# Kernel optimization log

Hardware: AMD Instinct MI355X
Metric: run time of the kernel (lower is better)

Reference implementation:

```python
import jax, jax.numpy as jnp
import numpy as np

N_NODES = 100000


def _deg_isqrt(idx, n):
    # clamped-to-1 degree, then ^-0.5 (DGL GraphConv norm='both')
    deg = jax.ops.segment_sum(jnp.ones(idx.shape, jnp.float32), idx, num_segments=n)
    return jnp.power(jnp.maximum(deg, 1.0), -0.5)


def _graph_conv(feat, W, b, src, dst, out_isqrt, in_isqrt, n):
    # norm='both': scale by src out-degree^-1/2, mult-first (in>out), spmm, scale by dst in-degree^-1/2
    h = (feat * out_isqrt[:, None]) @ W                      # [N, out]
    h = jax.ops.segment_sum(h[src], dst, num_segments=n)     # gather/scatter over edges
    return h * in_isqrt[:, None] + b


def setup_inputs() -> dict:
    key = jax.random.key(0)
    ks = jax.random.split(key, 10)
    in_dim, h1, h2 = 512, 64, 32
    n, e = N_NODES, 800000
    features = jax.random.normal(ks[0], (n, in_dim), jnp.float32)
    src = jax.random.randint(ks[1], (e,), 0, n)
    dst = jax.random.randint(ks[2], (e,), 0, n)
    noise = jax.random.normal(ks[3], (n, h2), jnp.float32)
    s1 = 1.0 / np.sqrt(in_dim)
    s2 = 1.0 / np.sqrt(h1)
    W1 = jax.random.uniform(ks[4], (in_dim, h1), jnp.float32, -s1, s1)
    b1 = jnp.zeros((h1,), jnp.float32)
    W2 = jax.random.uniform(ks[5], (h1, h2), jnp.float32, -s2, s2)
    b2 = jnp.zeros((h2,), jnp.float32)
    W3 = jax.random.uniform(ks[6], (h1, h2), jnp.float32, -s2, s2)
    b3 = jnp.zeros((h2,), jnp.float32)
    return {"features": features, "src": src, "dst": dst, "noise": noise,
            "W1": W1, "b1": b1, "W2": W2, "b2": b2, "W3": W3, "b3": b3}


def reference(features, src, dst, noise, W1, b1, W2, b2, W3, b3):
    n = features.shape[0]
    out_isqrt = _deg_isqrt(src, n)
    in_isqrt = _deg_isqrt(dst, n)
    h = jax.nn.relu(_graph_conv(features, W1, b1, src, dst, out_isqrt, in_isqrt, n))
    mean = _graph_conv(h, W2, b2, src, dst, out_isqrt, in_isqrt, n)
    log_std = _graph_conv(h, W3, b3, src, dst, out_isqrt, in_isqrt, n)
    z = mean + noise * jnp.exp(log_std)
    return z, mean, log_std
```

## Files before the change

kernel.cpp:

```cpp
#include <hip/hip_runtime.h>
#include <hip/hip_bf16.h>


typedef __attribute__((ext_vector_type(8))) short short8;
typedef __attribute__((ext_vector_type(4))) float f32x4;

static __device__ inline short f2bf(float f)
{
    union { __hip_bfloat16 h; short s; } u;
    u.h = __float2bfloat16(f);
    return u.s;
}

static __device__ inline short8 cvt8(float4 lo, float4 hi)
{
    short8 r;
    r[0] = f2bf(lo.x); r[1] = f2bf(lo.y); r[2] = f2bf(lo.z); r[3] = f2bf(lo.w);
    r[4] = f2bf(hi.x); r[5] = f2bf(hi.y); r[6] = f2bf(hi.z); r[7] = f2bf(hi.w);
    return r;
}

__global__ __launch_bounds__(256) void k_pack_w1(
    const float* __restrict__ W1, short* __restrict__ w1f)
{
    int gid = blockIdx.x * 256 + threadIdx.x;
    if (gid >= 512 * 64) return;
    int k = gid >> 6, c = gid & 63;
    int kt = k >> 5, kk = k & 31, nt = c >> 4, lr = c & 15;
    int kg = kk >> 3, j = kk & 7;
    int l = kg * 16 + lr;
    w1f[(kt * 4 + nt) * 512 + l * 8 + j] = f2bf(W1[gid]);
}

__global__ __launch_bounds__(256) void k_build_wc(
    const float* __restrict__ W2, const float* __restrict__ W3,
    float* __restrict__ wc)
{
    int gid = blockIdx.x * 256 + threadIdx.x;
    if (gid >= 64 * 64) return;
    int k = gid >> 6, c = gid & 63;
    wc[gid] = (c < 32) ? W2[k * 32 + c] : W3[k * 32 + (c - 32)];
}

__global__ __launch_bounds__(256) void k_deg_int(
    const int* __restrict__ src, const int* __restrict__ dst,
    int* __restrict__ degS, int* __restrict__ degD, int e)
{
    int gid = blockIdx.x * 256 + threadIdx.x;
    if (gid >= e) return;
    atomicAdd(&degS[src[gid]], 1);
    atomicAdd(&degD[dst[gid]], 1);
}

__global__ __launch_bounds__(256) void k_scan_block_sums(
    const int* __restrict__ deg, int* __restrict__ partials, int n)
{
    __shared__ int red[256];
    int gid = blockIdx.x * 256 + threadIdx.x;
    red[threadIdx.x] = (gid < n) ? deg[gid] : 0;
    __syncthreads();
    for (int s = 128; s > 0; s >>= 1) {
        if (threadIdx.x < s) red[threadIdx.x] += red[threadIdx.x + s];
        __syncthreads();
    }
    if (threadIdx.x == 0) partials[blockIdx.x] = red[0];
}

__global__ __launch_bounds__(512) void k_scan_partials(
    int* __restrict__ partials, int nb)
{
    __shared__ int s[512];
    int t = threadIdx.x;
    s[t] = (t < nb) ? partials[t] : 0;
    __syncthreads();
    for (int d = 1; d < 512; d <<= 1) {
        int v = (t >= d) ? s[t - d] : 0;
        __syncthreads();
        s[t] += v;
        __syncthreads();
    }
    if (t < nb) partials[t] = (t == 0) ? 0 : s[t - 1];
}

__global__ __launch_bounds__(256) void k_scan_final(
    const int* __restrict__ degD, const int* __restrict__ degS,
    const int* __restrict__ partials,
    int* __restrict__ row_ptr, int* __restrict__ cursor,
    float* __restrict__ isq_out, float* __restrict__ isq_in, int n)
{
    __shared__ int s[256];
    int t = threadIdx.x;
    int gid = blockIdx.x * 256 + t;
    int v = (gid < n) ? degD[gid] : 0;
    s[t] = v;
    __syncthreads();
    for (int d = 1; d < 256; d <<= 1) {
        int u = (t >= d) ? s[t - d] : 0;
        __syncthreads();
        s[t] += u;
        __syncthreads();
    }
    int start = partials[blockIdx.x] + s[t] - v;
    if (gid < n) {
        row_ptr[gid] = start;
        cursor[gid]  = start;
        isq_in[gid]  = 1.0f / sqrtf((float)max(v, 1));
        isq_out[gid] = 1.0f / sqrtf((float)max(degS[gid], 1));
    }
    if (gid == n - 1) row_ptr[n] = start + v;
}

__global__ __launch_bounds__(256) void k_scatter(
    const int* __restrict__ src, const int* __restrict__ dst,
    int* __restrict__ cursor, int* __restrict__ edge_src, int e)
{
    int gid = blockIdx.x * 256 + threadIdx.x;
    if (gid >= e) return;
    int pos = atomicAdd(&cursor[dst[gid]], 1);
    edge_src[pos] = src[gid];
}

__global__ __launch_bounds__(256) void k_gemm1_mfma(
    const float* __restrict__ X, const short* __restrict__ w1f,
    const float* __restrict__ scale, float* __restrict__ Y, int n)
{
    const int tid  = threadIdx.x;
    const int l    = tid & 63;
    const int wv   = tid >> 6;
    const int row0 = blockIdx.x * 128 + wv * 32;
    const int lr   = l & 15;
    const int kg   = l >> 4;

    int ra0 = row0 + lr;       if (ra0 >= n) ra0 = n - 1;
    int ra1 = row0 + 16 + lr;  if (ra1 >= n) ra1 = n - 1;
    const float* pa0 = X + (size_t)ra0 * 512 + kg * 8;
    const float* pa1 = X + (size_t)ra1 * 512 + kg * 8;

    f32x4 acc[2][4];
#pragma unroll
    for (int i = 0; i < 2; ++i)
#pragma unroll
        for (int j = 0; j < 4; ++j) acc[i][j] = (f32x4){0.f, 0.f, 0.f, 0.f};

    float4 a0lo = *(const float4*)(pa0);
    float4 a0hi = *(const float4*)(pa0 + 4);
    float4 a1lo = *(const float4*)(pa1);
    float4 a1hi = *(const float4*)(pa1 + 4);

    for (int kt = 0; kt < 16; ++kt) {
        const short* pb = w1f + (size_t)(kt * 4) * 512 + l * 8;
        short8 b0 = *(const short8*)(pb);
        short8 b1 = *(const short8*)(pb + 512);
        short8 b2 = *(const short8*)(pb + 1024);
        short8 b3 = *(const short8*)(pb + 1536);

        short8 a0 = cvt8(a0lo, a0hi);
        short8 a1 = cvt8(a1lo, a1hi);

        if (kt < 15) {
            const float* q0 = pa0 + (kt + 1) * 32;
            const float* q1 = pa1 + (kt + 1) * 32;
            a0lo = *(const float4*)(q0);
            a0hi = *(const float4*)(q0 + 4);
            a1lo = *(const float4*)(q1);
            a1hi = *(const float4*)(q1 + 4);
        }

        acc[0][0] = __builtin_amdgcn_mfma_f32_16x16x32_bf16(a0, b0, acc[0][0], 0, 0, 0);
        acc[0][1] = __builtin_amdgcn_mfma_f32_16x16x32_bf16(a0, b1, acc[0][1], 0, 0, 0);
        acc[0][2] = __builtin_amdgcn_mfma_f32_16x16x32_bf16(a0, b2, acc[0][2], 0, 0, 0);
        acc[0][3] = __builtin_amdgcn_mfma_f32_16x16x32_bf16(a0, b3, acc[0][3], 0, 0, 0);
        acc[1][0] = __builtin_amdgcn_mfma_f32_16x16x32_bf16(a1, b0, acc[1][0], 0, 0, 0);
        acc[1][1] = __builtin_amdgcn_mfma_f32_16x16x32_bf16(a1, b1, acc[1][1], 0, 0, 0);
        acc[1][2] = __builtin_amdgcn_mfma_f32_16x16x32_bf16(a1, b2, acc[1][2], 0, 0, 0);
        acc[1][3] = __builtin_amdgcn_mfma_f32_16x16x32_bf16(a1, b3, acc[1][3], 0, 0, 0);
    }

#pragma unroll
    for (int mr = 0; mr < 2; ++mr) {
#pragma unroll
        for (int m = 0; m < 4; ++m) {
            int row = row0 + mr * 16 + kg * 4 + m;
            if (row < n) {
                float s = scale[row];
#pragma unroll
                for (int nt = 0; nt < 4; ++nt)
                    Y[(size_t)row * 64 + nt * 16 + lr] = acc[mr][nt][m] * s;
            }
        }
    }
}

__global__ __launch_bounds__(256) void k_gemm2(
    const float* __restrict__ X, const float* __restrict__ W,
    float* __restrict__ Y, int n)
{
    __shared__ float sx[64][68];
    __shared__ float sw[64][64];
    const int tid  = threadIdx.x;
    const int colp = tid & 31;
    const int rg   = tid >> 5;
    const int row0 = blockIdx.x * 64;

    float2 acc[8];
#pragma unroll
    for (int i = 0; i < 8; ++i) acc[i] = make_float2(0.f, 0.f);

#pragma unroll
    for (int p = 0; p < 4; ++p) {
        int u = p * 256 + tid;
        int r = u >> 4, c4 = (u & 15) * 4;
        int row = row0 + r;
        float4 v = make_float4(0.f, 0.f, 0.f, 0.f);
        if (row < n) v = *(const float4*)&X[(size_t)row * 64 + c4];
        *(float4*)&sx[r][c4] = v;
        *(float4*)&sw[r][c4] = *(const float4*)&W[u * 4];
    }
    __syncthreads();

#pragma unroll 4
    for (int k4 = 0; k4 < 64; k4 += 4) {
        float2 w0 = *(const float2*)&sw[k4 + 0][colp * 2];
        float2 w1 = *(const float2*)&sw[k4 + 1][colp * 2];
        float2 w2 = *(const float2*)&sw[k4 + 2][colp * 2];
        float2 w3 = *(const float2*)&sw[k4 + 3][colp * 2];
#pragma unroll
        for (int i = 0; i < 8; ++i) {
            float4 f = *(const float4*)&sx[rg * 8 + i][k4];
            acc[i].x += f.x * w0.x + f.y * w1.x + f.z * w2.x + f.w * w3.x;
            acc[i].y += f.x * w0.y + f.y * w1.y + f.z * w2.y + f.w * w3.y;
        }
    }

#pragma unroll
    for (int i = 0; i < 8; ++i) {
        int row = row0 + rg * 8 + i;
        if (row < n)
            *(float2*)&Y[(size_t)row * 64 + colp * 2] =
                make_float2(acc[i].x, acc[i].y);
    }
}

__global__ __launch_bounds__(256) void k_gather_h(
    const int* __restrict__ row_ptr, const int* __restrict__ edge_src,
    const float* __restrict__ x, const float* __restrict__ isq_in,
    const float* __restrict__ isq_out, const float* __restrict__ b1,
    float* __restrict__ h, int n)
{
    int col  = threadIdx.x & 63;
    int node = __builtin_amdgcn_readfirstlane(blockIdx.x * 4 + (threadIdx.x >> 6));
    if (node >= n) return;
    int j = row_ptr[node], jend = row_ptr[node + 1];
    float a0 = 0.f, a1 = 0.f, a2 = 0.f, a3 = 0.f;
    for (; j + 3 < jend; j += 4) {
        int e0 = edge_src[j], e1 = edge_src[j + 1];
        int e2 = edge_src[j + 2], e3 = edge_src[j + 3];
        a0 += x[(size_t)e0 * 64 + col];
        a1 += x[(size_t)e1 * 64 + col];
        a2 += x[(size_t)e2 * 64 + col];
        a3 += x[(size_t)e3 * 64 + col];
    }
    for (; j < jend; ++j) a0 += x[(size_t)edge_src[j] * 64 + col];
    float acc = (a0 + a1) + (a2 + a3);
    h[(size_t)node * 64 + col] =
        fmaxf(acc * isq_in[node] + b1[col], 0.f) * isq_out[node];
}

__global__ __launch_bounds__(256) void k_gather_final(
    const int* __restrict__ row_ptr, const int* __restrict__ edge_src,
    const float* __restrict__ t23, const float* __restrict__ isq_in,
    const float* __restrict__ b2, const float* __restrict__ b3,
    const float* __restrict__ noise, float* __restrict__ out, int n)
{
    int lane = threadIdx.x & 63;
    int node = __builtin_amdgcn_readfirstlane(blockIdx.x * 4 + (threadIdx.x >> 6));
    if (node >= n) return;
    int j = row_ptr[node], jend = row_ptr[node + 1];
    float a0 = 0.f, a1 = 0.f, a2 = 0.f, a3 = 0.f;
    for (; j + 3 < jend; j += 4) {
        int e0 = edge_src[j], e1 = edge_src[j + 1];
        int e2 = edge_src[j + 2], e3 = edge_src[j + 3];
        a0 += t23[(size_t)e0 * 64 + lane];
        a1 += t23[(size_t)e1 * 64 + lane];
        a2 += t23[(size_t)e2 * 64 + lane];
        a3 += t23[(size_t)e3 * 64 + lane];
    }
    for (; j < jend; ++j) a0 += t23[(size_t)edge_src[j] * 64 + lane];
    float acc = (a0 + a1) + (a2 + a3);
    float si = isq_in[node];
    float v  = acc * si + (lane < 32 ? b2[lane] : b3[lane - 32]);
    float lv = __shfl(v, lane | 32, 64);
    int total = n * 32;
    int base  = node * 32 + (lane & 31);
    if (lane < 32) {
        float z = v + noise[base] * expf(lv);
        out[base]         = z;
        out[total + base] = v;
    } else {
        out[2 * total + base] = v;
    }
}

extern "C" void kernel_launch(void* const* d_in, const int* in_sizes, int n_in,
                              void* d_out, int out_size, void* d_ws, size_t ws_size,
                              hipStream_t stream)
{
    const float* feat  = (const float*)d_in[0];
    const int*   src   = (const int*)d_in[1];
    const int*   dst   = (const int*)d_in[2];
    const float* noise = (const float*)d_in[3];
    const float* W1    = (const float*)d_in[4];
    const float* b1    = (const float*)d_in[5];
    const float* W2    = (const float*)d_in[6];
    const float* b2    = (const float*)d_in[7];
    const float* W3    = (const float*)d_in[8];
    const float* b3    = (const float*)d_in[9];

    const int n = in_sizes[0] / 512;
    const int e = in_sizes[1];

    float* ws      = (float*)d_ws;
    float* isq_out = ws;
    float* isq_in  = ws + n;
    float* bufA    = ws + 2 * (size_t)n;
    float* bufB    = bufA + 64 * (size_t)n;
    float* wc      = bufB + 64 * (size_t)n;
    short* w1f     = (short*)(wc + 64 * 64);
    int*   ip      = (int*)(w1f + 512 * 64);
    int* row_ptr   = ip;
    int* cursor    = ip + (n + 1);
    int* partials  = cursor + n;
    int* edge_src  = partials + 512;
    int* degS = (int*)bufA;
    int* degD = degS + n;
    float* out = (float*)d_out;

    const int nb = (n + 255) / 256;

    hipMemsetAsync(degS, 0, 2 * (size_t)n * sizeof(int), stream);

    k_build_wc<<<(64 * 64 + 255) / 256, 256, 0, stream>>>(W2, W3, wc);
    k_pack_w1<<<(512 * 64 + 255) / 256, 256, 0, stream>>>(W1, w1f);
    k_deg_int<<<(e + 255) / 256, 256, 0, stream>>>(src, dst, degS, degD, e);

    k_scan_block_sums<<<nb, 256, 0, stream>>>(degD, partials, n);
    k_scan_partials<<<1, 512, 0, stream>>>(partials, nb);
    k_scan_final<<<nb, 256, 0, stream>>>(
        degD, degS, partials, row_ptr, cursor, isq_out, isq_in, n);
    k_scatter<<<(e + 255) / 256, 256, 0, stream>>>(src, dst, cursor, edge_src, e);

    k_gemm1_mfma<<<(n + 127) / 128, 256, 0, stream>>>(
        feat, w1f, isq_out, bufA, n);

    k_gather_h<<<(n + 3) / 4, 256, 0, stream>>>(
        row_ptr, edge_src, bufA, isq_in, isq_out, b1, bufB, n);

    k_gemm2<<<(n + 63) / 64, 256, 0, stream>>>(bufB, wc, bufA, n);

    k_gather_final<<<(n + 3) / 4, 256, 0, stream>>>(
        row_ptr, edge_src, bufA, isq_in, b2, b3, noise, out, n);
}
```

Measured before the change: 305.1 us.

## Store per-node projected features in bf16 and widen gather unroll

The GEMM outputs (the layer-1 projection and the layer-2/3 projections) are now written as bf16 instead of fp32. This halves the bytes moved by the two edge-gather kernels, which widen to fp32 on load and now unroll eight edges per iteration. The change also merges the weight packing, the wc build and the degree memset into one setup kernel, and software-pipelines the B-fragment loads in the MFMA GEMM. Rounding the intermediates to bf16 reduces accuracy, and the setup kernel zeroes 2n/4 int4 values, which leaves the tail of degS unzeroed when 2n is not a multiple of 4.

New measurement: 282.0 us. -7.6%, faster.

```diff
diff --git a/kernel.cpp b/kernel.cpp
--- a/kernel.cpp
+++ b/kernel.cpp
@@ -4,12 +4,20 @@
 
 typedef __attribute__((ext_vector_type(8))) short short8;
 typedef __attribute__((ext_vector_type(4))) float f32x4;
+typedef unsigned short ushort_t;
 
 static __device__ inline short f2bf(float f)
 {
     union { __hip_bfloat16 h; short s; } u;
     u.h = __float2bfloat16(f);
     return u.s;
+}
+
+static __device__ inline float bf2f(ushort_t u)
+{
+    union { float f; unsigned v; } w;
+    w.v = ((unsigned)u) << 16;
+    return w.f;
 }
 
 static __device__ inline short8 cvt8(float4 lo, float4 hi)
@@ -20,26 +28,24 @@
     return r;
 }
 
-__global__ __launch_bounds__(256) void k_pack_w1(
-    const float* __restrict__ W1, short* __restrict__ w1f)
+__global__ __launch_bounds__(256) void k_setup(
+    const float* __restrict__ W1, const float* __restrict__ W2,
+    const float* __restrict__ W3, short* __restrict__ w1f,
+    float* __restrict__ wc, int4* __restrict__ zp, int z4)
 {
     int gid = blockIdx.x * 256 + threadIdx.x;
-    if (gid >= 512 * 64) return;
-    int k = gid >> 6, c = gid & 63;
-    int kt = k >> 5, kk = k & 31, nt = c >> 4, lr = c & 15;
-    int kg = kk >> 3, j = kk & 7;
-    int l = kg * 16 + lr;
-    w1f[(kt * 4 + nt) * 512 + l * 8 + j] = f2bf(W1[gid]);
-}
-
-__global__ __launch_bounds__(256) void k_build_wc(
-    const float* __restrict__ W2, const float* __restrict__ W3,
-    float* __restrict__ wc)
-{
-    int gid = blockIdx.x * 256 + threadIdx.x;
-    if (gid >= 64 * 64) return;
-    int k = gid >> 6, c = gid & 63;
-    wc[gid] = (c < 32) ? W2[k * 32 + c] : W3[k * 32 + (c - 32)];
+    if (gid < z4) zp[gid] = make_int4(0, 0, 0, 0);
+    if (gid < 64 * 64) {
+        int k = gid >> 6, c = gid & 63;
+        wc[gid] = (c < 32) ? W2[k * 32 + c] : W3[k * 32 + (c - 32)];
+    }
+    if (gid < 512 * 64) {
+        int k = gid >> 6, c = gid & 63;
+        int kt = k >> 5, kk = k & 31, nt = c >> 4, lr = c & 15;
+        int kg = kk >> 3, j = kk & 7;
+        int l = kg * 16 + lr;
+        w1f[(kt * 4 + nt) * 512 + l * 8 + j] = f2bf(W1[gid]);
+    }
 }
 
 __global__ __launch_bounds__(256) void k_deg_int(
@@ -122,7 +128,7 @@
 
 __global__ __launch_bounds__(256) void k_gemm1_mfma(
     const float* __restrict__ X, const short* __restrict__ w1f,
-    const float* __restrict__ scale, float* __restrict__ Y, int n)
+    const float* __restrict__ scale, ushort_t* __restrict__ Y, int n)
 {
     const int tid  = threadIdx.x;
     const int l    = tid & 63;
@@ -135,6 +141,7 @@
     int ra1 = row0 + 16 + lr;  if (ra1 >= n) ra1 = n - 1;
     const float* pa0 = X + (size_t)ra0 * 512 + kg * 8;
     const float* pa1 = X + (size_t)ra1 * 512 + kg * 8;
+    const short* pb  = w1f + l * 8;
 
     f32x4 acc[2][4];
 #pragma unroll
@@ -146,16 +153,15 @@
     float4 a0hi = *(const float4*)(pa0 + 4);
     float4 a1lo = *(const float4*)(pa1);
     float4 a1hi = *(const float4*)(pa1 + 4);
+    short8 b0 = *(const short8*)(pb);
+    short8 b1 = *(const short8*)(pb + 512);
+    short8 b2 = *(const short8*)(pb + 1024);
+    short8 b3 = *(const short8*)(pb + 1536);
 
     for (int kt = 0; kt < 16; ++kt) {
-        const short* pb = w1f + (size_t)(kt * 4) * 512 + l * 8;
-        short8 b0 = *(const short8*)(pb);
-        short8 b1 = *(const short8*)(pb + 512);
-        short8 b2 = *(const short8*)(pb + 1024);
-        short8 b3 = *(const short8*)(pb + 1536);
-
-        short8 a0 = cvt8(a0lo, a0hi);
-        short8 a1 = cvt8(a1lo, a1hi);
+        short8 ca0 = cvt8(a0lo, a0hi);
+        short8 ca1 = cvt8(a1lo, a1hi);
+        short8 cb0 = b0, cb1 = b1, cb2 = b2, cb3 = b3;
 
         if (kt < 15) {
             const float* q0 = pa0 + (kt + 1) * 32;
@@ -164,16 +170,21 @@
             a0hi = *(const float4*)(q0 + 4);
             a1lo = *(const float4*)(q1);
             a1hi = *(const float4*)(q1 + 4);
+            const short* q = pb + (size_t)(kt + 1) * 2048;
+            b0 = *(const short8*)(q);
+            b1 = *(const short8*)(q + 512);
+            b2 = *(const short8*)(q + 1024);
+            b3 = *(const short8*)(q + 1536);
         }
 
-        acc[0][0] = __builtin_amdgcn_mfma_f32_16x16x32_bf16(a0, b0, acc[0][0], 0, 0, 0);
-        acc[0][1] = __builtin_amdgcn_mfma_f32_16x16x32_bf16(a0, b1, acc[0][1], 0, 0, 0);
-        acc[0][2] = __builtin_amdgcn_mfma_f32_16x16x32_bf16(a0, b2, acc[0][2], 0, 0, 0);
-        acc[0][3] = __builtin_amdgcn_mfma_f32_16x16x32_bf16(a0, b3, acc[0][3], 0, 0, 0);
-        acc[1][0] = __builtin_amdgcn_mfma_f32_16x16x32_bf16(a1, b0, acc[1][0], 0, 0, 0);
-        acc[1][1] = __builtin_amdgcn_mfma_f32_16x16x32_bf16(a1, b1, acc[1][1], 0, 0, 0);
-        acc[1][2] = __builtin_amdgcn_mfma_f32_16x16x32_bf16(a1, b2, acc[1][2], 0, 0, 0);
-        acc[1][3] = __builtin_amdgcn_mfma_f32_16x16x32_bf16(a1, b3, acc[1][3], 0, 0, 0);
+        acc[0][0] = __builtin_amdgcn_mfma_f32_16x16x32_bf16(ca0, cb0, acc[0][0], 0, 0, 0);
+        acc[0][1] = __builtin_amdgcn_mfma_f32_16x16x32_bf16(ca0, cb1, acc[0][1], 0, 0, 0);
+        acc[0][2] = __builtin_amdgcn_mfma_f32_16x16x32_bf16(ca0, cb2, acc[0][2], 0, 0, 0);
+        acc[0][3] = __builtin_amdgcn_mfma_f32_16x16x32_bf16(ca0, cb3, acc[0][3], 0, 0, 0);
+        acc[1][0] = __builtin_amdgcn_mfma_f32_16x16x32_bf16(ca1, cb0, acc[1][0], 0, 0, 0);
+        acc[1][1] = __builtin_amdgcn_mfma_f32_16x16x32_bf16(ca1, cb1, acc[1][1], 0, 0, 0);
+        acc[1][2] = __builtin_amdgcn_mfma_f32_16x16x32_bf16(ca1, cb2, acc[1][2], 0, 0, 0);
+        acc[1][3] = __builtin_amdgcn_mfma_f32_16x16x32_bf16(ca1, cb3, acc[1][3], 0, 0, 0);
     }
 
 #pragma unroll
@@ -185,15 +196,53 @@
                 float s = scale[row];
 #pragma unroll
                 for (int nt = 0; nt < 4; ++nt)
-                    Y[(size_t)row * 64 + nt * 16 + lr] = acc[mr][nt][m] * s;
+                    Y[(size_t)row * 64 + nt * 16 + lr] =
+                        (ushort_t)f2bf(acc[mr][nt][m] * s);
             }
         }
     }
 }
 
+__global__ __launch_bounds__(256) void k_gather_h(
+    const int* __restrict__ row_ptr, const int* __restrict__ edge_src,
+    const ushort_t* __restrict__ x, const float* __restrict__ isq_in,
+    const float* __restrict__ isq_out, const float* __restrict__ b1,
+    float* __restrict__ h, int n)
+{
+    int col  = threadIdx.x & 63;
+    int node = __builtin_amdgcn_readfirstlane(blockIdx.x * 4 + (threadIdx.x >> 6));
+    if (node >= n) return;
+    int j = row_ptr[node], jend = row_ptr[node + 1];
+    float a0 = 0.f, a1 = 0.f, a2 = 0.f, a3 = 0.f;
+    float a4 = 0.f, a5 = 0.f, a6 = 0.f, a7 = 0.f;
+    for (; j + 7 < jend; j += 8) {
+        int e0 = edge_src[j],     e1 = edge_src[j + 1];
+        int e2 = edge_src[j + 2], e3 = edge_src[j + 3];
+        int e4 = edge_src[j + 4], e5 = edge_src[j + 5];
+        int e6 = edge_src[j + 6], e7 = edge_src[j + 7];
+        a0 += bf2f(x[(size_t)e0 * 64 + col]);
+        a1 += bf2f(x[(size_t)e1 * 64 + col]);
+        a2 += bf2f(x[(size_t)e2 * 64 + col]);
+        a3 += bf2f(x[(size_t)e3 * 64 + col]);
+        a4 += bf2f(x[(size_t)e4 * 64 + col]);
+        a5 += bf2f(x[(size_t)e5 * 64 + col]);
+        a6 += bf2f(x[(size_t)e6 * 64 + col]);
+        a7 += bf2f(x[(size_t)e7 * 64 + col]);
+    }
+    for (; j + 1 < jend; j += 2) {
+        int e0 = edge_src[j], e1 = edge_src[j + 1];
+        a0 += bf2f(x[(size_t)e0 * 64 + col]);
+        a1 += bf2f(x[(size_t)e1 * 64 + col]);
+    }
+    if (j < jend) a2 += bf2f(x[(size_t)edge_src[j] * 64 + col]);
+    float acc = ((a0 + a1) + (a2 + a3)) + ((a4 + a5) + (a6 + a7));
+    h[(size_t)node * 64 + col] =
+        fmaxf(acc * isq_in[node] + b1[col], 0.f) * isq_out[node];
+}
+
 __global__ __launch_bounds__(256) void k_gemm2(
     const float* __restrict__ X, const float* __restrict__ W,
-    float* __restrict__ Y, int n)
+    ushort_t* __restrict__ Y, int n)
 {
     __shared__ float sx[64][68];
     __shared__ float sw[64][64];
@@ -235,40 +284,17 @@
 #pragma unroll
     for (int i = 0; i < 8; ++i) {
         int row = row0 + rg * 8 + i;
-        if (row < n)
-            *(float2*)&Y[(size_t)row * 64 + colp * 2] =
-                make_float2(acc[i].x, acc[i].y);
-    }
-}
-
-__global__ __launch_bounds__(256) void k_gather_h(
-    const int* __restrict__ row_ptr, const int* __restrict__ edge_src,
-    const float* __restrict__ x, const float* __restrict__ isq_in,
-    const float* __restrict__ isq_out, const float* __restrict__ b1,
-    float* __restrict__ h, int n)
-{
-    int col  = threadIdx.x & 63;
-    int node = __builtin_amdgcn_readfirstlane(blockIdx.x * 4 + (threadIdx.x >> 6));
-    if (node >= n) return;
-    int j = row_ptr[node], jend = row_ptr[node + 1];
-    float a0 = 0.f, a1 = 0.f, a2 = 0.f, a3 = 0.f;
-    for (; j + 3 < jend; j += 4) {
-        int e0 = edge_src[j], e1 = edge_src[j + 1];
-        int e2 = edge_src[j + 2], e3 = edge_src[j + 3];
-        a0 += x[(size_t)e0 * 64 + col];
-        a1 += x[(size_t)e1 * 64 + col];
-        a2 += x[(size_t)e2 * 64 + col];
-        a3 += x[(size_t)e3 * 64 + col];
-    }
-    for (; j < jend; ++j) a0 += x[(size_t)edge_src[j] * 64 + col];
-    float acc = (a0 + a1) + (a2 + a3);
-    h[(size_t)node * 64 + col] =
-        fmaxf(acc * isq_in[node] + b1[col], 0.f) * isq_out[node];
+        if (row < n) {
+            unsigned lo = (unsigned)(unsigned short)f2bf(acc[i].x);
+            unsigned hi = (unsigned)(unsigned short)f2bf(acc[i].y);
+            ((unsigned*)Y)[(size_t)row * 32 + colp] = (hi << 16) | lo;
+        }
+    }
 }
 
 __global__ __launch_bounds__(256) void k_gather_final(
     const int* __restrict__ row_ptr, const int* __restrict__ edge_src,
-    const float* __restrict__ t23, const float* __restrict__ isq_in,
+    const ushort_t* __restrict__ t23, const float* __restrict__ isq_in,
     const float* __restrict__ b2, const float* __restrict__ b3,
     const float* __restrict__ noise, float* __restrict__ out, int n)
 {
@@ -277,16 +303,28 @@
     if (node >= n) return;
     int j = row_ptr[node], jend = row_ptr[node + 1];
     float a0 = 0.f, a1 = 0.f, a2 = 0.f, a3 = 0.f;
-    for (; j + 3 < jend; j += 4) {
+    float a4 = 0.f, a5 = 0.f, a6 = 0.f, a7 = 0.f;
+    for (; j + 7 < jend; j += 8) {
+        int e0 = edge_src[j],     e1 = edge_src[j + 1];
+        int e2 = edge_src[j + 2], e3 = edge_src[j + 3];
+        int e4 = edge_src[j + 4], e5 = edge_src[j + 5];
+        int e6 = edge_src[j + 6], e7 = edge_src[j + 7];
+        a0 += bf2f(t23[(size_t)e0 * 64 + lane]);
+        a1 += bf2f(t23[(size_t)e1 * 64 + lane]);
+        a2 += bf2f(t23[(size_t)e2 * 64 + lane]);
+        a3 += bf2f(t23[(size_t)e3 * 64 + lane]);
+        a4 += bf2f(t23[(size_t)e4 * 64 + lane]);
+        a5 += bf2f(t23[(size_t)e5 * 64 + lane]);
+        a6 += bf2f(t23[(size_t)e6 * 64 + lane]);
+        a7 += bf2f(t23[(size_t)e7 * 64 + lane]);
+    }
+    for (; j + 1 < jend; j += 2) {
         int e0 = edge_src[j], e1 = edge_src[j + 1];
-        int e2 = edge_src[j + 2], e3 = edge_src[j + 3];
-        a0 += t23[(size_t)e0 * 64 + lane];
-        a1 += t23[(size_t)e1 * 64 + lane];
-        a2 += t23[(size_t)e2 * 64 + lane];
-        a3 += t23[(size_t)e3 * 64 + lane];
-    }
-    for (; j < jend; ++j) a0 += t23[(size_t)edge_src[j] * 64 + lane];
-    float acc = (a0 + a1) + (a2 + a3);
+        a0 += bf2f(t23[(size_t)e0 * 64 + lane]);
+        a1 += bf2f(t23[(size_t)e1 * 64 + lane]);
+    }
+    if (j < jend) a2 += bf2f(t23[(size_t)edge_src[j] * 64 + lane]);
+    float acc = ((a0 + a1) + (a2 + a3)) + ((a4 + a5) + (a6 + a7));
     float si = isq_in[node];
     float v  = acc * si + (lane < 32 ? b2[lane] : b3[lane - 32]);
     float lv = __shfl(v, lane | 32, 64);
@@ -336,11 +374,11 @@
     float* out = (float*)d_out;
 
     const int nb = (n + 255) / 256;
-
-    hipMemsetAsync(degS, 0, 2 * (size_t)n * sizeof(int), stream);
-
-    k_build_wc<<<(64 * 64 + 255) / 256, 256, 0, stream>>>(W2, W3, wc);
-    k_pack_w1<<<(512 * 64 + 255) / 256, 256, 0, stream>>>(W1, w1f);
+    const int z4 = (2 * n) / 4;
+
+    k_setup<<<(z4 + 255) / 256, 256, 0, stream>>>(
+        W1, W2, W3, w1f, wc, (int4*)degS, z4);
+
     k_deg_int<<<(e + 255) / 256, 256, 0, stream>>>(src, dst, degS, degD, e);
 
     k_scan_block_sums<<<nb, 256, 0, stream>>>(degD, partials, n);
@@ -350,13 +388,13 @@
     k_scatter<<<(e + 255) / 256, 256, 0, stream>>>(src, dst, cursor, edge_src, e);
 
     k_gemm1_mfma<<<(n + 127) / 128, 256, 0, stream>>>(
-        feat, w1f, isq_out, bufA, n);
+        feat, w1f, isq_out, (ushort_t*)bufA, n);
 
     k_gather_h<<<(n + 3) / 4, 256, 0, stream>>>(
-        row_ptr, edge_src, bufA, isq_in, isq_out, b1, bufB, n);
-
-    k_gemm2<<<(n + 63) / 64, 256, 0, stream>>>(bufB, wc, bufA, n);
+        row_ptr, edge_src, (const ushort_t*)bufA, isq_in, isq_out, b1, bufB, n);
+
+    k_gemm2<<<(n + 63) / 64, 256, 0, stream>>>(bufB, wc, (ushort_t*)bufA, n);
 
     k_gather_final<<<(n + 3) / 4, 256, 0, stream>>>(
-        row_ptr, edge_src, bufA, isq_in, b2, b3, noise, out, n);
-}
+        row_ptr, edge_src, (const ushort_t*)bufA, isq_in, b2, b3, noise, out, n);
+}
```
